# Optimization experiments

Hardware: AMD Instinct MI355X
Metric: run time of the kernel (lower is better)

## Reference

```python
import jax, jax.numpy as jnp
import numpy as np

N = 50000   # nodes
E = 400000  # edges
G = 256     # graphs in batch
D = 256     # out_dim (scalar channel width)
VD = 16     # vector channel width after v_emb


def setup_inputs() -> dict:
    key = jax.random.key(0)
    ks = jax.random.split(key, 12)

    def rn(k, shape, scale=0.02):
        return (jax.random.normal(k, shape) * scale).astype(jnp.float32)

    return dict(
        node_s=jax.random.normal(ks[0], (N, 23), jnp.float32),
        node_v=jax.random.normal(ks[1], (N, 4, 3), jnp.float32),
        edge_s=jax.random.normal(ks[2], (E, 17), jnp.float32),
        edge_index=jax.random.randint(ks[3], (2, E), 0, N, jnp.int32),
        batch=jnp.sort(jax.random.randint(ks[4], (N,), 0, G, jnp.int32)),
        Ws=rn(ks[5], (23, D)), bs=jnp.zeros((D,), jnp.float32),
        Wv=rn(ks[6], (4, VD)), bv=jnp.zeros((VD,), jnp.float32),
        We=rn(ks[7], (18, D)), be=jnp.zeros((D,), jnp.float32),
        Wm1=rn(ks[8], (2 * D + VD + D, D)), bm1=jnp.zeros((D,), jnp.float32),
        Wm2=rn(ks[9], (D, D)), bm2=jnp.zeros((D,), jnp.float32),
        Wn=rn(ks[10], (D + VD, D)), bn=jnp.zeros((D,), jnp.float32),
        gamma=jnp.ones((D,), jnp.float32), beta=jnp.zeros((D,), jnp.float32),
    )


def reference(node_s, node_v, edge_s, edge_index, batch,
              Ws, bs, Wv, bv, We, be, Wm1, bm1, Wm2, bm2, Wn, bn, gamma, beta):
    # --- embeddings ---
    s = node_s @ Ws + bs                                            # [N, D]
    e_in = jnp.concatenate([edge_s, jnp.zeros((edge_s.shape[0], 1), edge_s.dtype)], axis=-1)  # no edge_v branch
    e = e_in @ We + be                                              # [E, D]
    # v_emb: Linear over the 4 vector channels -> [N, VD, 3]
    v = jnp.einsum('nkc,ko->noc', node_v, Wv) + bv[None, :, None]
    v_norm = jnp.linalg.norm(v, axis=-1)                            # [N, VD]

    # --- SimpleGVPConv: gather -> 2-layer MLP per edge -> scatter-mean ---
    src, dst = edge_index[0], edge_index[1]                         # PyG: s_j = s[src], s_i = s[dst]
    m_in = jnp.concatenate([s[dst], s[src], v_norm[src], e], axis=-1)  # [E, 2D+VD+D]
    m = jax.nn.relu(m_in @ Wm1 + bm1) @ Wm2 + bm2                   # [E, D]
    agg = jax.ops.segment_sum(m, dst, num_segments=N)               # [N, D]
    cnt = jax.ops.segment_sum(jnp.ones((E,), m.dtype), dst, num_segments=N)
    s = s + agg / jnp.maximum(cnt, 1.0)[:, None]                    # mean aggr + residual update

    # --- node MLP: Linear -> LayerNorm -> ReLU (dropout = eval identity) ---
    feat = jnp.concatenate([s, v_norm], axis=-1)                    # [N, D+VD]
    h = feat @ Wn + bn                                              # [N, D]
    mu = h.mean(axis=-1, keepdims=True)
    var = h.var(axis=-1, keepdims=True)
    h = (h - mu) * jax.lax.rsqrt(var + 1e-5) * gamma + beta
    h = jax.nn.relu(h)

    # --- global mean pool ---
    gsum = jax.ops.segment_sum(h, batch, num_segments=G)            # [G, D]
    gcnt = jax.ops.segment_sum(jnp.ones((h.shape[0],), h.dtype), batch, num_segments=G)
    return gsum / jnp.maximum(gcnt, 1.0)[:, None]
```

## Files before the change

kernel.cpp:

```cpp
#include <hip/hip_runtime.h>
#include <hip/hip_bf16.h>

typedef unsigned short u16;
typedef __attribute__((ext_vector_type(8))) short short8;
typedef __attribute__((ext_vector_type(4))) short short4v;
typedef __attribute__((ext_vector_type(4))) float f32x4;

#define NN 50000
#define EE 400000
#define GG 256
#define MP 50048
#define KS 64
#define K2 320
#define EWS 260

static __device__ __forceinline__ __hip_bfloat16 f2b(float x) { return __float2bfloat16(x); }
static __device__ __forceinline__ float u16tof(u16 v) {
    unsigned x = ((unsigned)v) << 16;
    float f;
    __builtin_memcpy(&f, &x, 4);
    return f;
}
static __device__ __forceinline__ u16 ftou16(float x) {
    __hip_bfloat16 h = __float2bfloat16(x);
    u16 b;
    __builtin_memcpy(&b, &h, 2);
    return b;
}

static __device__ __forceinline__ float dot256(const float* __restrict__ a,
                                               const float* __restrict__ b, int c) {
    const float* __restrict__ bp = b + c;
    float s0 = 0.f, s1 = 0.f, s2 = 0.f, s3 = 0.f;
    float s4 = 0.f, s5 = 0.f, s6 = 0.f, s7 = 0.f;
#pragma unroll 4
    for (int j = 0; j < 256; j += 8) {
        s0 += a[j]     * bp[(size_t)(j)     * 256];
        s1 += a[j + 1] * bp[(size_t)(j + 1) * 256];
        s2 += a[j + 2] * bp[(size_t)(j + 2) * 256];
        s3 += a[j + 3] * bp[(size_t)(j + 3) * 256];
        s4 += a[j + 4] * bp[(size_t)(j + 4) * 256];
        s5 += a[j + 5] * bp[(size_t)(j + 5) * 256];
        s6 += a[j + 6] * bp[(size_t)(j + 6) * 256];
        s7 += a[j + 7] * bp[(size_t)(j + 7) * 256];
    }
    return ((s0 + s1) + (s2 + s3)) + ((s4 + s5) + (s6 + s7));
}

__global__ __launch_bounds__(256) void phase1(const float* __restrict__ Wm1,
                                              const float* __restrict__ Wn,
                                              const float* __restrict__ Wm2,
                                              const float* __restrict__ We,
                                              const float* __restrict__ be,
                                              const float* __restrict__ bm1,
                                              const float* __restrict__ bm2,
                                              const float* __restrict__ Ws,
                                              const float* __restrict__ bs,
                                              __hip_bfloat16* __restrict__ W1pqT,
                                              __hip_bfloat16* __restrict__ W2T,
                                              float* __restrict__ Wc, float* __restrict__ bc,
                                              float* __restrict__ crow,
                                              const float* __restrict__ node_s,
                                              const float* __restrict__ node_v,
                                              const float* __restrict__ Wv,
                                              const float* __restrict__ bv,
                                              __hip_bfloat16* __restrict__ XL2,
                                              const int* __restrict__ ei,
                                              const int* __restrict__ batch,
                                              int* __restrict__ cnt,
                                              int* __restrict__ gstart) {
    int blk = blockIdx.x, tid = threadIdx.x;
    if (blk < 64) {
        int k = blk;
#pragma unroll
        for (int half = 0; half < 2; ++half) {
            int c = half * 256 + tid;
            int cc = c & 255;
            const float* Wm1h = (c < 256) ? Wm1 : (Wm1 + 256 * 256);
            float v = 0.f;
            if (k < 23) v = dot256(&Ws[k * 256], Wm1h, cc);
            else if (k < 39) { if (c >= 256) v = Wm1[(512 + (k - 23)) * 256 + cc]; }
            else if (k == 39) v = dot256(bs, Wm1h, cc);
            W1pqT[c * KS + k] = f2b(v);
        }
    } else if (blk < 384) {
        int k = blk - 64, c = tid;
        float v = 0.f;
        if (k < 23) v = dot256(&Ws[k * 256], Wn, c);
        else if (k < 39) v = Wn[(256 + (k - 23)) * 256 + c];
        else if (k == 39) v = dot256(bs, Wn, c);
        else if (k < 296) v = dot256(&Wm2[(k - 40) * 256], Wn, c);
        W2T[c * K2 + k] = f2b(v);
    } else if (blk < 403) {
        int b = blk - 384, c = tid;
        if (b < 17) Wc[b * 256 + c] = dot256(&We[b * 256], &Wm1[528 * 256], c);
        else if (b == 17) bc[c] = bm1[c] + dot256(be, &Wm1[528 * 256], c);
        else crow[c] = dot256(bm2, Wn, c);
    } else if (blk < 12903) {
        int w = tid >> 6, lane = tid & 63;
        int n = (blk - 403) * 4 + w;
        if (n < NN) {
            float lv = (lane < 23) ? node_s[(size_t)n * 23 + lane] : 0.f;
            float vv = (lane < 12) ? node_v[(size_t)n * 12 + lane] : 0.f;
            float nvk[12];
#pragma unroll
            for (int k = 0; k < 12; ++k) nvk[k] = __shfl(vv, k, 64);
            float vn = 0.f;
            if (lane < 16) {
                float b0 = bv[lane];
                float vx = b0, vy = b0, vz = b0;
#pragma unroll
                for (int k = 0; k < 4; ++k) {
                    float wv = Wv[k * 16 + lane];
                    vx += nvk[k * 3 + 0] * wv;
                    vy += nvk[k * 3 + 1] * wv;
                    vz += nvk[k * 3 + 2] * wv;
                }
                vn = sqrtf(vx * vx + vy * vy + vz * vz);
            }
            int vsrc = (lane >= 23 && lane < 39) ? (lane - 23) : 0;
            float vbc = __shfl(vn, vsrc, 64);
            float outv;
            if (lane < 23) outv = lv;
            else if (lane < 39) outv = vbc;
            else if (lane == 39) outv = 1.f;
            else outv = 0.f;
            __hip_bfloat16* row = XL2 + (size_t)n * K2;
            row[lane] = f2b(outv);
            if (lane < 24) row[296 + lane] = f2b(0.f);
        }
    } else if (blk < 14466) {
        int e = (blk - 12903) * 256 + tid;
        if (e < EE) atomicAdd(&cnt[ei[EE + e]], 1);
    } else {
        int n = (blk - 14466) * 256 + tid;
        if (n < NN) {
            int bn = batch[n];
            int bp = (n == 0) ? -1 : batch[n - 1];
            for (int g = bp + 1; g <= bn; ++g) gstart[g] = n;
            if (n == NN - 1)
                for (int g = bn + 1; g <= GG; ++g) gstart[g] = NN;
        }
    }
}

__global__ __launch_bounds__(256) void scan1(const int* __restrict__ cnt, int* __restrict__ rowptr,
                                             int* __restrict__ bsum) {
    int tid = threadIdx.x, i = blockIdx.x * 256 + tid;
    __shared__ int sd[256];
    int v = (i < NN) ? cnt[i] : 0;
    sd[tid] = v;
    __syncthreads();
    for (int off = 1; off < 256; off <<= 1) {
        int t = (tid >= off) ? sd[tid - off] : 0;
        __syncthreads();
        sd[tid] += t;
        __syncthreads();
    }
    if (i < NN) rowptr[i] = sd[tid] - v;
    if (tid == 255) bsum[blockIdx.x] = sd[255];
}
__global__ __launch_bounds__(256) void scan2(int* __restrict__ bsum, const int* __restrict__ gstart,
                                             float* __restrict__ ginv) {
    int c = threadIdx.x;
    __shared__ int sd[256];
    int v = (c < 196) ? bsum[c] : 0;
    sd[c] = v;
    __syncthreads();
    for (int off = 1; off < 256; off <<= 1) {
        int t = (c >= off) ? sd[c - off] : 0;
        __syncthreads();
        sd[c] += t;
        __syncthreads();
    }
    if (c < 196) bsum[c] = sd[c] - v;
    ginv[c] = 1.f / fmaxf((float)(gstart[c + 1] - gstart[c]), 1.f);
}
__global__ __launch_bounds__(256) void scan3(const int* __restrict__ cnt, const int* __restrict__ bsum,
                                             int* __restrict__ rowptr, int* __restrict__ cursor) {
    int i = blockIdx.x * 256 + threadIdx.x;
    if (i < NN) {
        int v = rowptr[i] + bsum[blockIdx.x];
        rowptr[i] = v;
        cursor[i] = v;
        if (i == NN - 1) rowptr[NN] = v + cnt[i];
    }
}

__global__ __launch_bounds__(256, 2) void gemm1_fill(const u16* __restrict__ A, const u16* __restrict__ Bt,
                                                     __hip_bfloat16* __restrict__ C,
                                                     const int* __restrict__ ei, int* __restrict__ cursor,
                                                     int* __restrict__ eid, int* __restrict__ srcv,
                                                     const float* __restrict__ Wc,
                                                     u16* __restrict__ WcBf) {
    __shared__ __align__(16) u16 At[128 * 64];
    __shared__ __align__(16) u16 Bs[128 * 64];
    int blk = blockIdx.x, tid = threadIdx.x;
    if (blk >= 1564) {
        if (blk == 3127) {
            for (int idx = tid; idx < 8192; idx += 256) {
                int ni = idx >> 9;
                int l = (idx >> 3) & 63;
                int j = idx & 7;
                int k = ((l >> 4) << 3) + j;
                int c = ni * 16 + (l & 15);
                float v = (k < 17) ? Wc[k * 256 + c] : 0.f;
                WcBf[idx] = ftou16(v);
            }
            return;
        }
        int e = (blk - 1564) * 256 + tid;
        if (e < EE) {
            int d = ei[EE + e];
            int s = ei[e];
            int pos = atomicAdd(&cursor[d], 1);
            eid[pos] = e;
            srcv[pos] = s;
        }
        return;
    }
    long m0 = (long)(blk >> 2) * 128;
    long n0 = (long)(blk & 3) * 128;
    int wid = tid >> 6, lane = tid & 63;
    int wm = wid >> 1, wn = wid & 1;
    int quad = lane >> 4, l16 = lane & 15;
    f32x4 acc[4][4] = {};
    int r0 = tid >> 3;
    int cc = (tid & 7) * 8;
    const u16* Ab = A + (m0 + r0) * K2 + cc;
    const u16* Bb = Bt + (n0 + r0) * KS + cc;
#pragma unroll
    for (int i = 0; i < 4; ++i) {
        int row = r0 + i * 32;
        __builtin_amdgcn_global_load_lds(
            (const __attribute__((address_space(1))) void*)(Ab + (long)(i * 32) * K2),
            (__attribute__((address_space(3))) void*)(&At[row * 64 + cc]), 16, 0, 0);
    }
#pragma unroll
    for (int i = 0; i < 4; ++i) {
        int row = r0 + i * 32;
        __builtin_amdgcn_global_load_lds(
            (const __attribute__((address_space(1))) void*)(Bb + (long)(i * 32) * KS),
            (__attribute__((address_space(3))) void*)(&Bs[row * 64 + cc]), 16, 0, 0);
    }
    __syncthreads();
#pragma unroll
    for (int kk = 0; kk < 64; kk += 32) {
        short8 af[4], bf[4];
#pragma unroll
        for (int mi = 0; mi < 4; ++mi)
            af[mi] = *(const short8*)&At[(wm * 64 + mi * 16 + l16) * 64 + kk + quad * 8];
#pragma unroll
        for (int ni = 0; ni < 4; ++ni)
            bf[ni] = *(const short8*)&Bs[(wn * 64 + ni * 16 + l16) * 64 + kk + quad * 8];
#pragma unroll
        for (int mi = 0; mi < 4; ++mi) {
#pragma unroll
            for (int ni = 0; ni < 4; ++ni)
                acc[mi][ni] = __builtin_amdgcn_mfma_f32_16x16x32_bf16(af[mi], bf[ni], acc[mi][ni], 0, 0, 0);
        }
    }
#pragma unroll
    for (int mi = 0; mi < 4; ++mi) {
#pragma unroll
        for (int ni = 0; ni < 4; ++ni) {
            long row = m0 + wm * 64 + mi * 16 + quad * 4;
            long col = n0 + wn * 64 + ni * 16 + l16;
#pragma unroll
            for (int r = 0; r < 4; ++r)
                C[(row + r) * 512 + col] = f2b(acc[mi][ni][r]);
        }
    }
}

__global__ __launch_bounds__(128) void edge_agg(const u16* __restrict__ PQ,
                                                const float* __restrict__ edge_s,
                                                const int* __restrict__ srcv,
                                                const int* __restrict__ eid,
                                                const int* __restrict__ rowptr,
                                                const u16* __restrict__ WcBf,
                                                const float* __restrict__ bc,
                                                __hip_bfloat16* __restrict__ XL2) {
    __shared__ __align__(16) u16 EWall[2][16 * EWS];
    int tid = threadIdx.x;
    int wv = tid >> 6, lane = tid & 63;
    int n = blockIdx.x * 2 + wv;
    if (n >= NN) return;
    u16* __restrict__ EW = &EWall[wv][0];
    int start = rowptr[n], deg = rowptr[n + 1] - start;
    int l16 = lane & 15, quad = lane >> 4;
    short8 wcf[16];
#pragma unroll
    for (int ni = 0; ni < 16; ++ni)
        wcf[ni] = *(const short8*)&WcBf[ni * 512 + lane * 8];
    f32x4 bc4 = *(const f32x4*)&bc[lane * 4];
    short4v p4 = *(const short4v*)&PQ[(size_t)n * 512 + lane * 4];
    f32x4 pb;
#pragma unroll
    for (int i = 0; i < 4; ++i) pb[i] = u16tof((u16)p4[i]) + bc4[i];
    f32x4 acc = {0.f, 0.f, 0.f, 0.f};
    const f32x4 zf = {0.f, 0.f, 0.f, 0.f};
    for (int base = 0; base < deg; base += 64) {
        int m = deg - base;
        if (m > 64) m = 64;
        int mm1 = m - 1;
        int ee = 0, ss = 0;
        if (lane < m) {
            ee = eid[start + base + lane];
            ss = srcv[start + base + lane];
        }
        auto loadQ = [&](int p) {
            int pc = (p < mm1) ? p : mm1;
            int s = __builtin_amdgcn_readlane(ss, pc);
            return *(const short4v*)&PQ[(size_t)s * 512 + 256 + lane * 4];
        };
        int ng = (m + 15) >> 4;
        for (int g = 0; g < ng; ++g) {
            int b16 = g * 16;
            short4v qA0 = loadQ(b16 + 0);
            short4v qA1 = loadQ(b16 + 1);
            short4v qA2 = loadQ(b16 + 2);
            short4v qA3 = loadQ(b16 + 3);
            short4v qA4 = loadQ(b16 + 4);
            short4v qA5 = loadQ(b16 + 5);
            short4v qA6 = loadQ(b16 + 6);
            short4v qA7 = loadQ(b16 + 7);
            int li = b16 + l16;
            if (li > mm1) li = mm1;
            int ev = __shfl(ee, li, 64);
            const float* ep = edge_s + (size_t)ev * 17 + quad * 8;
            float a0 = 0.f, a1 = 0.f, a2 = 0.f, a3 = 0.f, a4 = 0.f, a5 = 0.f, a6 = 0.f, a7 = 0.f;
            if (quad < 2) {
                a0 = ep[0]; a1 = ep[1]; a2 = ep[2]; a3 = ep[3];
                a4 = ep[4]; a5 = ep[5]; a6 = ep[6]; a7 = ep[7];
            } else if (quad == 2) {
                a0 = ep[0];
            }
            short8 af;
            af[0] = (short)ftou16(a0); af[1] = (short)ftou16(a1);
            af[2] = (short)ftou16(a2); af[3] = (short)ftou16(a3);
            af[4] = (short)ftou16(a4); af[5] = (short)ftou16(a5);
            af[6] = (short)ftou16(a6); af[7] = (short)ftou16(a7);
#pragma unroll
            for (int ni = 0; ni < 16; ++ni) {
                f32x4 ew = __builtin_amdgcn_mfma_f32_16x16x32_bf16(af, wcf[ni], zf, 0, 0, 0);
#pragma unroll
                for (int r = 0; r < 4; ++r)
                    EW[(quad * 4 + r) * EWS + ni * 16 + l16] = ftou16(ew[r]);
            }
            short4v qB0 = loadQ(b16 + 8);
            short4v qB1 = loadQ(b16 + 9);
            short4v qB2 = loadQ(b16 + 10);
            short4v qB3 = loadQ(b16 + 11);
            short4v qB4 = loadQ(b16 + 12);
            short4v qB5 = loadQ(b16 + 13);
            short4v qB6 = loadQ(b16 + 14);
            short4v qB7 = loadQ(b16 + 15);
            int mg = m - b16;
            if (mg > 16) mg = 16;
#define CONSUME(QQ, c)                                                              \
            {                                                                       \
                int jj = (c);                                                       \
                if (jj < mg) {                                                      \
                    short4v ew4 = *(const short4v*)&EW[jj * EWS + lane * 4];        \
                    _Pragma("unroll")                                               \
                    for (int i = 0; i < 4; ++i)                                     \
                        acc[i] += fmaxf(pb[i] + u16tof((u16)QQ[i]) +                \
                                        u16tof((u16)ew4[i]), 0.f);                  \
                }                                                                   \
            }
            CONSUME(qA0, 0)  CONSUME(qA1, 1)  CONSUME(qA2, 2)  CONSUME(qA3, 3)
            CONSUME(qA4, 4)  CONSUME(qA5, 5)  CONSUME(qA6, 6)  CONSUME(qA7, 7)
            CONSUME(qB0, 8)  CONSUME(qB1, 9)  CONSUME(qB2, 10) CONSUME(qB3, 11)
            CONSUME(qB4, 12) CONSUME(qB5, 13) CONSUME(qB6, 14) CONSUME(qB7, 15)
#undef CONSUME
        }
    }
    float inv = 1.f / fmaxf((float)deg, 1.f);
    short4v ov;
#pragma unroll
    for (int i = 0; i < 4; ++i) ov[i] = (short)ftou16(acc[i] * inv);
    *(short4v*)&XL2[(size_t)n * K2 + 40 + lane * 4] = ov;
}

__global__ __launch_bounds__(256, 2) void gemm2_lnp(const u16* __restrict__ A, const u16* __restrict__ Bt,
                                                    const int* __restrict__ cnt, const int* __restrict__ batch,
                                                    const float* __restrict__ bn, const float* __restrict__ crow,
                                                    const float* __restrict__ gamma, const float* __restrict__ beta,
                                                    const float* __restrict__ ginv, float* __restrict__ out) {
    __shared__ __align__(16) u16 At[64 * 64];
    __shared__ __align__(16) u16 Bs[256 * 64];
    __shared__ float rsum[4][64], rsum2[4][64];
    __shared__ int sdeg[64], sbatch[64];
    int tid = threadIdx.x;
    long m0 = (long)blockIdx.x * 64;
    int w = tid >> 6, lane = tid & 63;
    int quad = lane >> 4, l16 = lane & 15;
    f32x4 acc[4][4] = {};
    int r0 = tid >> 3;
    int cc = (tid & 7) * 8;
    const u16* Ab = A + (m0 + r0) * K2 + cc;
    const u16* Bb = Bt + (long)r0 * K2 + cc;
    for (int kt = 0; kt < K2; kt += 64) {
#pragma unroll
        for (int i = 0; i < 2; ++i) {
            int row = r0 + i * 32;
            __builtin_amdgcn_global_load_lds(
                (const __attribute__((address_space(1))) void*)(Ab + (long)(i * 32) * K2 + kt),
                (__attribute__((address_space(3))) void*)(&At[row * 64 + cc]), 16, 0, 0);
        }
#pragma unroll
        for (int i = 0; i < 8; ++i) {
            int row = r0 + i * 32;
            __builtin_amdgcn_global_load_lds(
                (const __attribute__((address_space(1))) void*)(Bb + (long)(i * 32) * K2 + kt),
                (__attribute__((address_space(3))) void*)(&Bs[row * 64 + cc]), 16, 0, 0);
        }
        __syncthreads();
#pragma unroll
        for (int kk = 0; kk < 64; kk += 32) {
            short8 af[4], bf[4];
#pragma unroll
            for (int mi = 0; mi < 4; ++mi)
                af[mi] = *(const short8*)&At[(mi * 16 + l16) * 64 + kk + quad * 8];
#pragma unroll
            for (int ni = 0; ni < 4; ++ni)
                bf[ni] = *(const short8*)&Bs[(w * 64 + ni * 16 + l16) * 64 + kk + quad * 8];
#pragma unroll
            for (int mi = 0; mi < 4; ++mi) {
#pragma unroll
                for (int ni = 0; ni < 4; ++ni)
                    acc[mi][ni] = __builtin_amdgcn_mfma_f32_16x16x32_bf16(af[mi], bf[ni], acc[mi][ni], 0, 0, 0);
            }
        }
        __syncthreads();
    }
    if (tid < 64) {
        long n = m0 + tid;
        sdeg[tid] = (n < NN) ? cnt[n] : 0;
        sbatch[tid] = (n < NN) ? batch[n] : -1;
    }
    __syncthreads();
    float bn_l[4], cr_l[4], g_l[4], be_l[4];
#pragma unroll
    for (int ni = 0; ni < 4; ++ni) {
        int col = w * 64 + ni * 16 + l16;
        bn_l[ni] = bn[col];
        cr_l[ni] = crow[col];
        g_l[ni] = gamma[col];
        be_l[ni] = beta[col];
    }
#pragma unroll
    for (int mi = 0; mi < 4; ++mi) {
#pragma unroll
        for (int r = 0; r < 4; ++r) {
            int row = mi * 16 + quad * 4 + r;
            float cr_on = (sdeg[row] > 0) ? 1.f : 0.f;
            float s = 0.f, s2 = 0.f;
#pragma unroll
            for (int ni = 0; ni < 4; ++ni) {
                float xv = acc[mi][ni][r] + bn_l[ni] + cr_on * cr_l[ni];
                acc[mi][ni][r] = xv;
                s += xv;
                s2 += xv * xv;
            }
            s += __shfl_xor(s, 1, 64);  s2 += __shfl_xor(s2, 1, 64);
            s += __shfl_xor(s, 2, 64);  s2 += __shfl_xor(s2, 2, 64);
            s += __shfl_xor(s, 4, 64);  s2 += __shfl_xor(s2, 4, 64);
            s += __shfl_xor(s, 8, 64);  s2 += __shfl_xor(s2, 8, 64);
            if (l16 == 0) { rsum[w][row] = s; rsum2[w][row] = s2; }
        }
    }
    __syncthreads();
    float mu_a[4][4], rs_a[4][4];
#pragma unroll
    for (int mi = 0; mi < 4; ++mi) {
#pragma unroll
        for (int r = 0; r < 4; ++r) {
            int row = mi * 16 + quad * 4 + r;
            float S = rsum[0][row] + rsum[1][row] + rsum[2][row] + rsum[3][row];
            float S2 = rsum2[0][row] + rsum2[1][row] + rsum2[2][row] + rsum2[3][row];
            float mu = S * (1.f / 256.f);
            mu_a[mi][r] = mu;
            rs_a[mi][r] = rsqrtf(S2 * (1.f / 256.f) - mu * mu + 1e-5f);
        }
    }
#pragma unroll
    for (int ni = 0; ni < 4; ++ni) {
        int col = w * 64 + ni * 16 + l16;
        float pacc = 0.f;
        int curg = -1;
#pragma unroll
        for (int mi = 0; mi < 4; ++mi) {
#pragma unroll
            for (int r = 0; r < 4; ++r) {
                int row = mi * 16 + quad * 4 + r;
                int g = sbatch[row];
                float y = (acc[mi][ni][r] - mu_a[mi][r]) * rs_a[mi][r] * g_l[ni] + be_l[ni];
                y = fmaxf(y, 0.f);
                if (g != curg) {
                    if (curg >= 0) atomicAdd(&out[curg * 256 + col], pacc * ginv[curg]);
                    pacc = 0.f;
                    curg = g;
                }
                if (g >= 0) pacc += y;
            }
        }
        if (curg >= 0) atomicAdd(&out[curg * 256 + col], pacc * ginv[curg]);
    }
}

extern "C" void kernel_launch(void* const* d_in, const int* in_sizes, int n_in,
                              void* d_out, int out_size, void* d_ws, size_t ws_size,
                              hipStream_t stream) {
    const float* node_s = (const float*)d_in[0];
    const float* node_v = (const float*)d_in[1];
    const float* edge_s = (const float*)d_in[2];
    const int* ei = (const int*)d_in[3];
    const int* batch = (const int*)d_in[4];
    const float* Ws = (const float*)d_in[5];
    const float* bs = (const float*)d_in[6];
    const float* Wv = (const float*)d_in[7];
    const float* bv = (const float*)d_in[8];
    const float* We = (const float*)d_in[9];
    const float* be = (const float*)d_in[10];
    const float* Wm1 = (const float*)d_in[11];
    const float* bm1 = (const float*)d_in[12];
    const float* Wm2 = (const float*)d_in[13];
    const float* bm2 = (const float*)d_in[14];
    const float* Wn = (const float*)d_in[15];
    const float* bn = (const float*)d_in[16];
    const float* gamma = (const float*)d_in[17];
    const float* beta = (const float*)d_in[18];

    char* ws = (char*)d_ws;
    size_t off = 0;
    auto take = [&](size_t n) {
        void* p = ws + off;
        off = (off + n + 255) & ~(size_t)255;
        return p;
    };
    __hip_bfloat16* XL2 = (__hip_bfloat16*)take((size_t)MP * K2 * 2);
    __hip_bfloat16* PQ = (__hip_bfloat16*)take((size_t)MP * 512 * 2);
    __hip_bfloat16* W1pqT = (__hip_bfloat16*)take(512 * KS * 2);
    __hip_bfloat16* W2T = (__hip_bfloat16*)take(256 * K2 * 2);
    float* Wc = (float*)take(17 * 256 * 4);
    float* bc = (float*)take(256 * 4);
    float* crow = (float*)take(256 * 4);
    u16* WcBf = (u16*)take(16 * 512 * 2);
    int* cnt = (int*)take(NN * 4);
    int* gstart = (int*)take((GG + 1) * 4);
    float* ginv = (float*)take(GG * 4);
    int* rowptr = (int*)take((NN + 1) * 4);
    int* cursor = (int*)take(NN * 4);
    int* eid = (int*)take(EE * 4);
    int* srcv = (int*)take(EE * 4);
    int* bsum = (int*)take(256 * 4);

    hipMemsetAsync(cnt, 0, NN * 4, stream);
    hipMemsetAsync(d_out, 0, (size_t)out_size * 4, stream);

    phase1<<<14662, 256, 0, stream>>>(Wm1, Wn, Wm2, We, be, bm1, bm2, Ws, bs,
                                      W1pqT, W2T, Wc, bc, crow,
                                      node_s, node_v, Wv, bv, XL2, ei, batch, cnt, gstart);

    scan1<<<196, 256, 0, stream>>>(cnt, rowptr, bsum);
    scan2<<<1, 256, 0, stream>>>(bsum, gstart, ginv);
    scan3<<<196, 256, 0, stream>>>(cnt, bsum, rowptr, cursor);

    gemm1_fill<<<3128, 256, 0, stream>>>((const u16*)XL2, (const u16*)W1pqT, PQ, ei, cursor, eid,
                                         srcv, Wc, WcBf);

    edge_agg<<<25000, 128, 0, stream>>>((const u16*)PQ, edge_s, srcv, eid, rowptr, WcBf, bc, XL2);

    gemm2_lnp<<<782, 256, 0, stream>>>((const u16*)XL2, (const u16*)W2T, cnt, batch,
                                       bn, crow, gamma, beta, ginv, (float*)d_out);
}
```

Before: 309.4 us.

## Fold weights with MFMA, run edge_agg one wave per block, skip unused Q loads

The W2T weight-folding step (Ws/bs/Wm2 times Wn) drops its 320 scalar dot-product blocks and uses 10 blocks doing bf16 MFMA tiles, which cuts phase1's block count. edge_agg now launches one 64-thread block per node instead of packing two nodes per 128-thread block, so a wave with a short degree list no longer sits in a block with a longer one. The second group of eight Q gathers is loaded only when more than eight edges remain. The folded weights are now computed from bf16-rounded inputs, which may change precision slightly.

New measurement: 291.0 us. 6.0% less time.

```diff
diff --git a/kernel.cpp b/kernel.cpp
--- a/kernel.cpp
+++ b/kernel.cpp
@@ -83,22 +83,71 @@
             else if (k == 39) v = dot256(bs, Wm1h, cc);
             W1pqT[c * KS + k] = f2b(v);
         }
-    } else if (blk < 384) {
-        int k = blk - 64, c = tid;
-        float v = 0.f;
-        if (k < 23) v = dot256(&Ws[k * 256], Wn, c);
-        else if (k < 39) v = Wn[(256 + (k - 23)) * 256 + c];
-        else if (k == 39) v = dot256(bs, Wn, c);
-        else if (k < 296) v = dot256(&Wm2[(k - 40) * 256], Wn, c);
-        W2T[c * K2 + k] = f2b(v);
-    } else if (blk < 403) {
-        int b = blk - 384, c = tid;
+    } else if (blk < 74) {
+        int wb = blk - 64;
+        int kt0 = (wb >> 1) * 64;
+        int c0 = (wb & 1) * 128;
+        int w = tid >> 6, lane = tid & 63;
+        int quad = lane >> 4, l16 = lane & 15;
+        f32x4 acc[4][2] = {};
+        for (int jt = 0; jt < 256; jt += 32) {
+            int j0 = jt + quad * 8;
+            short8 af[4], bf[2];
+#pragma unroll
+            for (int mi = 0; mi < 4; ++mi) {
+                int k = kt0 + mi * 16 + l16;
+                const float* ar = nullptr;
+                if (k < 23) ar = Ws + (size_t)k * 256;
+                else if (k == 39) ar = bs;
+                else if (k >= 40 && k < 296) ar = Wm2 + (size_t)(k - 40) * 256;
+                float v0 = 0.f, v1 = 0.f, v2 = 0.f, v3 = 0.f, v4 = 0.f, v5 = 0.f, v6 = 0.f, v7 = 0.f;
+                if (ar) {
+                    f32x4 x0 = *(const f32x4*)(ar + j0);
+                    f32x4 x1 = *(const f32x4*)(ar + j0 + 4);
+                    v0 = x0[0]; v1 = x0[1]; v2 = x0[2]; v3 = x0[3];
+                    v4 = x1[0]; v5 = x1[1]; v6 = x1[2]; v7 = x1[3];
+                }
+                af[mi][0] = (short)ftou16(v0); af[mi][1] = (short)ftou16(v1);
+                af[mi][2] = (short)ftou16(v2); af[mi][3] = (short)ftou16(v3);
+                af[mi][4] = (short)ftou16(v4); af[mi][5] = (short)ftou16(v5);
+                af[mi][6] = (short)ftou16(v6); af[mi][7] = (short)ftou16(v7);
+            }
+#pragma unroll
+            for (int ni = 0; ni < 2; ++ni) {
+                int c = c0 + w * 32 + ni * 16 + l16;
+#pragma unroll
+                for (int u = 0; u < 8; ++u)
+                    bf[ni][u] = (short)ftou16(Wn[(size_t)(j0 + u) * 256 + c]);
+            }
+#pragma unroll
+            for (int mi = 0; mi < 4; ++mi) {
+#pragma unroll
+                for (int ni = 0; ni < 2; ++ni)
+                    acc[mi][ni] = __builtin_amdgcn_mfma_f32_16x16x32_bf16(af[mi], bf[ni], acc[mi][ni], 0, 0, 0);
+            }
+        }
+#pragma unroll
+        for (int mi = 0; mi < 4; ++mi) {
+#pragma unroll
+            for (int ni = 0; ni < 2; ++ni) {
+                int c = c0 + w * 32 + ni * 16 + l16;
+#pragma unroll
+                for (int r = 0; r < 4; ++r) {
+                    int k = kt0 + mi * 16 + quad * 4 + r;
+                    float v = acc[mi][ni][r];
+                    if (k >= 23 && k < 39) v = Wn[(size_t)(256 + k - 23) * 256 + c];
+                    W2T[(size_t)c * K2 + k] = f2b(v);
+                }
+            }
+        }
+    } else if (blk < 93) {
+        int b = blk - 74, c = tid;
         if (b < 17) Wc[b * 256 + c] = dot256(&We[b * 256], &Wm1[528 * 256], c);
         else if (b == 17) bc[c] = bm1[c] + dot256(be, &Wm1[528 * 256], c);
         else crow[c] = dot256(bm2, Wn, c);
-    } else if (blk < 12903) {
+    } else if (blk < 12593) {
         int w = tid >> 6, lane = tid & 63;
-        int n = (blk - 403) * 4 + w;
+        int n = (blk - 93) * 4 + w;
         if (n < NN) {
             float lv = (lane < 23) ? node_s[(size_t)n * 23 + lane] : 0.f;
             float vv = (lane < 12) ? node_v[(size_t)n * 12 + lane] : 0.f;
@@ -129,11 +178,11 @@
             row[lane] = f2b(outv);
             if (lane < 24) row[296 + lane] = f2b(0.f);
         }
-    } else if (blk < 14466) {
-        int e = (blk - 12903) * 256 + tid;
+    } else if (blk < 14156) {
+        int e = (blk - 12593) * 256 + tid;
         if (e < EE) atomicAdd(&cnt[ei[EE + e]], 1);
     } else {
-        int n = (blk - 14466) * 256 + tid;
+        int n = (blk - 14156) * 256 + tid;
         if (n < NN) {
             int bn = batch[n];
             int bp = (n == 0) ? -1 : batch[n - 1];
@@ -273,20 +322,17 @@
     }
 }
 
-__global__ __launch_bounds__(128) void edge_agg(const u16* __restrict__ PQ,
-                                                const float* __restrict__ edge_s,
-                                                const int* __restrict__ srcv,
-                                                const int* __restrict__ eid,
-                                                const int* __restrict__ rowptr,
-                                                const u16* __restrict__ WcBf,
-                                                const float* __restrict__ bc,
-                                                __hip_bfloat16* __restrict__ XL2) {
-    __shared__ __align__(16) u16 EWall[2][16 * EWS];
-    int tid = threadIdx.x;
-    int wv = tid >> 6, lane = tid & 63;
-    int n = blockIdx.x * 2 + wv;
-    if (n >= NN) return;
-    u16* __restrict__ EW = &EWall[wv][0];
+__global__ __launch_bounds__(64) void edge_agg(const u16* __restrict__ PQ,
+                                               const float* __restrict__ edge_s,
+                                               const int* __restrict__ srcv,
+                                               const int* __restrict__ eid,
+                                               const int* __restrict__ rowptr,
+                                               const u16* __restrict__ WcBf,
+                                               const float* __restrict__ bc,
+                                               __hip_bfloat16* __restrict__ XL2) {
+    __shared__ __align__(16) u16 EW[16 * EWS];
+    int lane = threadIdx.x;
+    int n = blockIdx.x;
     int start = rowptr[n], deg = rowptr[n + 1] - start;
     int l16 = lane & 15, quad = lane >> 4;
     short8 wcf[16];
@@ -348,16 +394,20 @@
                 for (int r = 0; r < 4; ++r)
                     EW[(quad * 4 + r) * EWS + ni * 16 + l16] = ftou16(ew[r]);
             }
-            short4v qB0 = loadQ(b16 + 8);
-            short4v qB1 = loadQ(b16 + 9);
-            short4v qB2 = loadQ(b16 + 10);
-            short4v qB3 = loadQ(b16 + 11);
-            short4v qB4 = loadQ(b16 + 12);
-            short4v qB5 = loadQ(b16 + 13);
-            short4v qB6 = loadQ(b16 + 14);
-            short4v qB7 = loadQ(b16 + 15);
             int mg = m - b16;
             if (mg > 16) mg = 16;
+            short4v qB0 = {0, 0, 0, 0}, qB1 = {0, 0, 0, 0}, qB2 = {0, 0, 0, 0}, qB3 = {0, 0, 0, 0};
+            short4v qB4 = {0, 0, 0, 0}, qB5 = {0, 0, 0, 0}, qB6 = {0, 0, 0, 0}, qB7 = {0, 0, 0, 0};
+            if (mg > 8) {
+                qB0 = loadQ(b16 + 8);
+                qB1 = loadQ(b16 + 9);
+                qB2 = loadQ(b16 + 10);
+                qB3 = loadQ(b16 + 11);
+                qB4 = loadQ(b16 + 12);
+                qB5 = loadQ(b16 + 13);
+                qB6 = loadQ(b16 + 14);
+                qB7 = loadQ(b16 + 15);
+            }
 #define CONSUME(QQ, c)                                                              \
             {                                                                       \
                 int jj = (c);                                                       \
@@ -560,7 +610,7 @@
     hipMemsetAsync(cnt, 0, NN * 4, stream);
     hipMemsetAsync(d_out, 0, (size_t)out_size * 4, stream);
 
-    phase1<<<14662, 256, 0, stream>>>(Wm1, Wn, Wm2, We, be, bm1, bm2, Ws, bs,
+    phase1<<<14352, 256, 0, stream>>>(Wm1, Wn, Wm2, We, be, bm1, bm2, Ws, bs,
                                       W1pqT, W2T, Wc, bc, crow,
                                       node_s, node_v, Wv, bv, XL2, ei, batch, cnt, gstart);
 
@@ -571,7 +621,7 @@
     gemm1_fill<<<3128, 256, 0, stream>>>((const u16*)XL2, (const u16*)W1pqT, PQ, ei, cursor, eid,
                                          srcv, Wc, WcBf);
 
-    edge_agg<<<25000, 128, 0, stream>>>((const u16*)PQ, edge_s, srcv, eid, rowptr, WcBf, bc, XL2);
+    edge_agg<<<NN, 64, 0, stream>>>((const u16*)PQ, edge_s, srcv, eid, rowptr, WcBf, bc, XL2);
 
     gemm2_lnp<<<782, 256, 0, stream>>>((const u16*)XL2, (const u16*)W2T, cnt, batch,
                                        bn, crow, gamma, beta, ginv, (float*)d_out);
```
